# Optimization experiments

Hardware: AMD Instinct MI355X
Metric: run time of the kernel (lower is better)

Reference implementation:

```python
import jax, jax.numpy as jnp
import numpy as np

D = 1024
B = 16384

def setup_inputs() -> dict:
    key = jax.random.key(0)
    ks = jax.random.split(key, 8)
    s = 1.0 / np.sqrt(D)  # torch Linear default init scale (uniform), use scaled normal
    return {
        "f1": jax.random.normal(ks[0], (B, D), jnp.float32),
        "f2": jax.random.normal(ks[1], (B, D), jnp.float32),
        "Wq": jax.random.normal(ks[2], (D, D), jnp.float32) * s,
        "bq": jax.random.normal(ks[3], (D,), jnp.float32) * s,
        "Wk": jax.random.normal(ks[4], (D, D), jnp.float32) * s,
        "bk": jax.random.normal(ks[5], (D,), jnp.float32) * s,
        "Wv": jax.random.normal(ks[6], (D, D), jnp.float32) * s,
        "bv": jax.random.normal(ks[7], (D,), jnp.float32) * s,
    }

def reference(f1, f2, Wq, bq, Wk, bk, Wv, bv):
    d = f1.shape[-1]
    feats = jnp.stack([f1, f2], axis=1)          # [B, 2, D]
    # nn.Linear: y = x @ W.T + b
    Q = jnp.einsum("bsd,ed->bse", feats, Wq) + bq  # [B, 2, D]
    K = jnp.einsum("bsd,ed->bse", feats, Wk) + bk
    V = jnp.einsum("bsd,ed->bse", feats, Wv) + bv
    scores = jnp.einsum("bse,bte->bst", Q, K) / jnp.sqrt(jnp.asarray(d, feats.dtype))  # [B, 2, 2]
    attn = jax.nn.softmax(scores, axis=-1)
    attended = jnp.einsum("bst,btd->bsd", attn, V)  # [B, 2, D]
    return attended.sum(axis=1)                     # [B, D]
```

## Files before the change

kernel.cpp:

```cpp
#include <hip/hip_runtime.h>
#include <hip/hip_bf16.h>
#include <stdint.h>

typedef unsigned short u16;
typedef __bf16 bf16x8 __attribute__((ext_vector_type(8)));
typedef float f32x4 __attribute__((ext_vector_type(4)));

#define D_DIM 1024
#define B_ROWS 16384
#define M_ROWS 32768
#define BM 128
#define BN 128
#define BK 64

__device__ __forceinline__ u16 f2bs(float f) {
    union { float f; unsigned u; } v; v.f = f;
    unsigned r = v.u + 0x7FFFu + ((v.u >> 16) & 1u);
    return (u16)(r >> 16);
}
__device__ __forceinline__ float bs2f(unsigned bits16) {
    union { unsigned u; float f; } v; v.u = bits16 << 16;
    return v.f;
}
__device__ __forceinline__ float b8x(uint4 q, int e) {
    unsigned w[4] = {q.x, q.y, q.z, q.w};
    return bs2f((w[e >> 1] >> ((unsigned)(e & 1) * 16u)) & 0xFFFFu);
}
__device__ __forceinline__ uint2 pack4(float4 f) {
    uint2 r;
    r.x = (unsigned)f2bs(f.x) | ((unsigned)f2bs(f.y) << 16);
    r.y = (unsigned)f2bs(f.z) | ((unsigned)f2bs(f.w) << 16);
    return r;
}

#define GLD16(gsrc, ldst)                                                      \
    __builtin_amdgcn_global_load_lds(                                          \
        (const __attribute__((address_space(1))) void*)(gsrc),                 \
        (__attribute__((address_space(3))) void*)(ldst), 16, 0, 0)

#define MFMA16(a, b, c) __builtin_amdgcn_mfma_f32_16x16x32_bf16((a), (b), (c), 0, 0, 0)

__global__ __launch_bounds__(256) void prep_all(const float* __restrict__ f1,
                                                const float* __restrict__ f2,
                                                const float* __restrict__ Wq,
                                                const float* __restrict__ Wk,
                                                const float* __restrict__ Wv,
                                                const float* __restrict__ bq,
                                                const float* __restrict__ bk,
                                                u16* __restrict__ X,
                                                u16* __restrict__ WqT,
                                                u16* __restrict__ WkT,
                                                u16* __restrict__ Wvb,
                                                float* __restrict__ u,
                                                float* __restrict__ v,
                                                float* __restrict__ cbuf) {
    const int bid = blockIdx.x;
    if (bid < 2048) {
        const float* in = (bid < 1024) ? Wq : Wk;
        u16* out = (bid < 1024) ? WqT : WkT;
        const int b = bid & 1023;
        __shared__ float lds[32][33];
        const int tx = threadIdx.x & 31;
        const int ty = threadIdx.x >> 5;
        const int r0 = (b >> 5) * 32;
        const int c0 = (b & 31) * 32;
#pragma unroll
        for (int i = 0; i < 4; ++i) {
            int r = ty + i * 8;
            lds[r][tx] = in[(size_t)(r0 + r) * D_DIM + c0 + tx];
        }
        __syncthreads();
#pragma unroll
        for (int i = 0; i < 4; ++i) {
            int r = ty + i * 8;
            out[(size_t)(c0 + r) * D_DIM + r0 + tx] = f2bs(lds[tx][r]);
        }
    } else if (bid < 3072) {
        size_t base = ((size_t)(bid - 2048) * 256 + threadIdx.x) * 4;
        *(uint2*)(Wvb + base) = pack4(*(const float4*)(Wv + base));
    } else if (bid < 3104) {
        const int b = bid - 3072;
        const int dl = threadIdx.x & 31;
        const int fg = threadIdx.x >> 5;
        const int d  = b * 32 + dl;
        float au = 0.f, av = 0.f;
        const int f0 = fg * 128;
        for (int f = f0; f < f0 + 128; ++f) {
            au = fmaf(Wq[(size_t)f * D_DIM + d], bk[f], au);
            av = fmaf(Wk[(size_t)f * D_DIM + d], bq[f], av);
        }
        __shared__ float su[8][32], sv[8][32];
        su[fg][dl] = au; sv[fg][dl] = av;
        __syncthreads();
        if (fg == 0) {
            float a = 0.f, b2 = 0.f;
#pragma unroll
            for (int g = 0; g < 8; ++g) { a += su[g][dl]; b2 += sv[g][dl]; }
            u[d] = a; v[d] = b2;
        }
        if (b == 0) {
            __shared__ float red[256];
            float p = 0.f;
            for (int f = threadIdx.x; f < D_DIM; f += 256) p = fmaf(bq[f], bk[f], p);
            red[threadIdx.x] = p;
            __syncthreads();
            for (int s = 128; s; s >>= 1) {
                if (threadIdx.x < s) red[threadIdx.x] += red[threadIdx.x + s];
                __syncthreads();
            }
            if (threadIdx.x == 0) cbuf[0] = red[0];
        }
    } else {
        size_t i4   = (size_t)(bid - 3104) * 256 + threadIdx.x;
        size_t base = i4 * 4;
        size_t brow = base >> 10;
        size_t col  = base & 1023;
        float4 a = *(const float4*)(f1 + base);
        float4 b = *(const float4*)(f2 + base);
        *(uint2*)(X + (2 * brow) * D_DIM + col)     = pack4(a);
        *(uint2*)(X + (2 * brow + 1) * D_DIM + col) = pack4(b);
    }
}

__global__ __launch_bounds__(256, 3) void gemm_small(const u16* __restrict__ A,
                                                     const u16* __restrict__ W,
                                                     u16* __restrict__ C, int ncols) {
    constexpr int K = D_DIM;
    __shared__ u16 As[BM * BK];
    __shared__ u16 Bs[BN * BK];

    const int cpx  = gridDim.x >> 3;
    const int orig = (blockIdx.x & 7) * cpx + (blockIdx.x >> 3);
    const int nTn = ncols / BN;
    const int m0 = (orig / nTn) * BM, n0 = (orig % nTn) * BN;

    const int tid  = threadIdx.x;
    const int lane = tid & 63;
    const int wave = tid >> 6;
    const int wr = wave >> 1, wc = wave & 1;
    const int lr = lane & 15;
    const int kg = lane >> 4;

    f32x4 acc[4][4] = {};

    const int sr  = tid >> 3;
    const int scs = ((tid & 7) ^ ((tid >> 3) & 7)) * 8;
    const u16* aRow = A + (size_t)(m0 + sr) * K + scs;
    const u16* bRow = W + (size_t)(n0 + sr) * K + scs;
    u16* aDst = As + tid * 8;
    u16* bDst = Bs + tid * 8;

    for (int kt = 0; kt < K; kt += BK) {
#pragma unroll
        for (int i = 0; i < 4; ++i) {
            GLD16(aRow + (size_t)i * 32 * K + kt, aDst + i * 2048);
            GLD16(bRow + (size_t)i * 32 * K + kt, bDst + i * 2048);
        }
        __syncthreads();
#pragma unroll
        for (int kk = 0; kk < 2; ++kk) {
            bf16x8 af[4], bfr[4];
            const int kx = kk * 4 + kg;
#pragma unroll
            for (int mf = 0; mf < 4; ++mf) {
                const int R = wr * 64 + mf * 16 + lr;
                af[mf] = *(const bf16x8*)(As + R * 64 + ((kx ^ (R & 7)) * 8));
            }
#pragma unroll
            for (int nf = 0; nf < 4; ++nf) {
                const int S = wc * 64 + nf * 16 + lr;
                bfr[nf] = *(const bf16x8*)(Bs + S * 64 + ((kx ^ (S & 7)) * 8));
            }
#pragma unroll
            for (int mf = 0; mf < 4; ++mf)
#pragma unroll
                for (int nf = 0; nf < 4; ++nf)
                    acc[mf][nf] = MFMA16(af[mf], bfr[nf], acc[mf][nf]);
        }
        __syncthreads();
    }

    const int cr = (lane >> 4) * 4;
    const int cc = lane & 15;
#pragma unroll
    for (int mf = 0; mf < 4; ++mf)
#pragma unroll
        for (int nf = 0; nf < 4; ++nf) {
            int col = n0 + wc * 64 + nf * 16 + cc;
#pragma unroll
            for (int j = 0; j < 4; ++j) {
                int row = m0 + wr * 64 + mf * 16 + cr + j;
                C[(size_t)row * ncols + col] = f2bs(acc[mf][nf][j]);
            }
        }
}

template<int MODE>
__global__ __launch_bounds__(512, 2) void gemm8p(const u16* __restrict__ A,
                                                 const u16* __restrict__ W,
                                                 const float* __restrict__ bias,
                                                 u16* __restrict__ C,
                                                 float* __restrict__ out,
                                                 int ncols) {
    constexpr int K  = D_DIM;
    constexpr int NT = K / 64;
    __shared__ u16 L[65536];

    const int cpx  = gridDim.x >> 3;
    const int orig = (blockIdx.x & 7) * cpx + (blockIdx.x >> 3);
    const int nTn  = ncols >> 8;
    const int m0 = (orig / nTn) << 8, n0 = (orig % nTn) << 8;

    const int tid  = threadIdx.x;
    const int lane = tid & 63;
    const int wid  = tid >> 6;
    const int wm = wid >> 2, wn = wid & 3;
    const int lr = lane & 15;
    const int kg = lane >> 4;
    const int r7 = lr & 7;
    const int cx0 = ((0 + kg) ^ r7) * 8;
    const int cx1 = ((4 + kg) ^ r7) * 8;
    const int sS  = (wn & 1) * 64;

    const int rb  = tid >> 3;
    const int scs = ((tid & 7) ^ (rb & 7)) * 8;
    const u16* aB = A + (size_t)(m0 + rb) * K + scs;
    const u16* bB = W + (size_t)(n0 + rb) * K + scs;
    u16* aD = L + tid * 8;
    u16* bD = L + 32768 + tid * 8;

#define ST_HALF(tile, h)                                                       \
    {                                                                          \
        const int d_ = (tile) & 1;                                             \
        const size_t ko_ = (size_t)(tile) * 64;                                \
        if ((h) < 2) {                                                         \
            const u16* s_ = aB + (size_t)(h) * 128 * K + ko_;                  \
            u16* t_ = aD + (d_ * 2 + (h)) * 8192;                              \
            GLD16(s_, t_);                                                     \
            GLD16(s_ + (size_t)64 * K, t_ + 4096);                            \
        } else {                                                               \
            const u16* s_ = bB + (size_t)((h) - 2) * 128 * K + ko_;            \
            u16* t_ = bD + (d_ * 2 + ((h) - 2)) * 8192;                        \
            GLD16(s_, t_);                                                     \
            GLD16(s_ + (size_t)64 * K, t_ + 4096);                            \
        }                                                                      \
    }

    f32x4 acc[8][4] = {};
    bf16x8 af[8][2], bf[4][2];

#pragma unroll
    for (int h = 0; h < 4; ++h) ST_HALF(0, h);
#pragma unroll
    for (int h = 0; h < 4; ++h) ST_HALF(1, h);
    asm volatile("s_waitcnt vmcnt(8)" ::: "memory");
    __builtin_amdgcn_s_barrier();

#pragma unroll 2
    for (int t = 0; t < NT; ++t) {
        const int d = t & 1;
        const u16* Ab = L + (d * 2 + wm) * 8192;
        const u16* Bb = L + 32768 + (d * 2 + (wn >> 1)) * 8192;
        const bool more = (t + 2 < NT);

#pragma unroll
        for (int m = 0; m < 4; ++m) {
            const int R = m * 16 + lr;
            af[m][0] = *(const bf16x8*)(Ab + R * 64 + cx0);
            af[m][1] = *(const bf16x8*)(Ab + R * 64 + cx1);
        }
#pragma unroll
        for (int n = 0; n < 2; ++n) {
            const int S = sS + n * 16 + lr;
            bf[n][0] = *(const bf16x8*)(Bb + S * 64 + cx0);
            bf[n][1] = *(const bf16x8*)(Bb + S * 64 + cx1);
        }
        __builtin_amdgcn_s_barrier();
        __builtin_amdgcn_s_setprio(1);
#pragma unroll
        for (int m = 0; m < 4; ++m)
#pragma unroll
            for (int n = 0; n < 2; ++n) {
                acc[m][n] = MFMA16(af[m][0], bf[n][0], acc[m][n]);
                acc[m][n] = MFMA16(af[m][1], bf[n][1], acc[m][n]);
            }
        __builtin_amdgcn_s_setprio(0);
        __builtin_amdgcn_s_barrier();

#pragma unroll
        for (int n = 2; n < 4; ++n) {
            const int S = sS + n * 16 + lr;
            bf[n][0] = *(const bf16x8*)(Bb + S * 64 + cx0);
            bf[n][1] = *(const bf16x8*)(Bb + S * 64 + cx1);
        }
        __builtin_amdgcn_s_barrier();
        __builtin_amdgcn_s_setprio(1);
#pragma unroll
        for (int m = 0; m < 4; ++m)
#pragma unroll
            for (int n = 2; n < 4; ++n) {
                acc[m][n] = MFMA16(af[m][0], bf[n][0], acc[m][n]);
                acc[m][n] = MFMA16(af[m][1], bf[n][1], acc[m][n]);
            }
        __builtin_amdgcn_s_setprio(0);
        __builtin_amdgcn_s_barrier();

#pragma unroll
        for (int m = 4; m < 8; ++m) {
            const int R = m * 16 + lr;
            af[m][0] = *(const bf16x8*)(Ab + R * 64 + cx0);
            af[m][1] = *(const bf16x8*)(Ab + R * 64 + cx1);
        }
        if (more) { ST_HALF(t + 2, 2); ST_HALF(t + 2, 3); }
        __builtin_amdgcn_s_barrier();
        __builtin_amdgcn_s_setprio(1);
#pragma unroll
        for (int m = 4; m < 8; ++m)
#pragma unroll
            for (int n = 0; n < 2; ++n) {
                acc[m][n] = MFMA16(af[m][0], bf[n][0], acc[m][n]);
                acc[m][n] = MFMA16(af[m][1], bf[n][1], acc[m][n]);
            }
        __builtin_amdgcn_s_setprio(0);
        __builtin_amdgcn_s_barrier();

        if (more) { ST_HALF(t + 2, 0); ST_HALF(t + 2, 1); }
        __builtin_amdgcn_s_barrier();
        __builtin_amdgcn_s_setprio(1);
#pragma unroll
        for (int m = 4; m < 8; ++m)
#pragma unroll
            for (int n = 2; n < 4; ++n) {
                acc[m][n] = MFMA16(af[m][0], bf[n][0], acc[m][n]);
                acc[m][n] = MFMA16(af[m][1], bf[n][1], acc[m][n]);
            }
        __builtin_amdgcn_s_setprio(0);
        if (more) asm volatile("s_waitcnt vmcnt(8)" ::: "memory");
        else      asm volatile("s_waitcnt vmcnt(0)" ::: "memory");
        __builtin_amdgcn_s_barrier();
    }
#undef ST_HALF

    const int cr = (lane >> 4) * 4;
    const int cc = lane & 15;
    if constexpr (MODE == 0) {
#pragma unroll
        for (int mf = 0; mf < 8; ++mf)
#pragma unroll
            for (int nf = 0; nf < 4; ++nf) {
                int col = n0 + wn * 64 + nf * 16 + cc;
#pragma unroll
                for (int j = 0; j < 4; ++j) {
                    int row = m0 + wm * 128 + mf * 16 + cr + j;
                    C[(size_t)row * ncols + col] = f2bs(acc[mf][nf][j]);
                }
            }
    } else {
#pragma unroll
        for (int mf = 0; mf < 8; ++mf)
#pragma unroll
            for (int nf = 0; nf < 4; ++nf) {
                int col = n0 + wn * 64 + nf * 16 + cc;
                float bsv = 2.0f * bias[col];
#pragma unroll
                for (int j = 0; j < 4; ++j) {
                    int row = m0 + wm * 128 + mf * 16 + cr + j;
                    out[(size_t)row * ncols + col] = acc[mf][nf][j] + bsv;
                }
            }
    }
}

__global__ __launch_bounds__(256) void scores_z(const u16* __restrict__ X,
                                                const u16* __restrict__ G,
                                                const float* __restrict__ u,
                                                const float* __restrict__ v,
                                                const float* __restrict__ cbuf,
                                                u16* __restrict__ Z) {
    const int wave = threadIdx.x >> 6;
    const int lane = threadIdx.x & 63;
    const size_t b = (size_t)blockIdx.x * 4 + wave;
    const u16* x0p = X + (2 * b) * D_DIM;
    const u16* x1p = x0p + D_DIM;
    const u16* g0p = G + (2 * b) * D_DIM;
    const u16* g1p = g0p + D_DIM;

    float d00 = 0.f, d01 = 0.f, d10 = 0.f, d11 = 0.f;
    float au0 = 0.f, au1 = 0.f, bv0 = 0.f, bv1 = 0.f;
    uint4 x0c[2], x1c[2];
#pragma unroll
    for (int s = 0; s < 2; ++s) {
        const int c = s * 512 + lane * 8;
        x0c[s] = *(const uint4*)(x0p + c);
        x1c[s] = *(const uint4*)(x1p + c);
        uint4 g0 = *(const uint4*)(g0p + c);
        uint4 g1 = *(const uint4*)(g1p + c);
        float4 uuA = *(const float4*)(u + c);
        float4 uuB = *(const float4*)(u + c + 4);
        float4 vvA = *(const float4*)(v + c);
        float4 vvB = *(const float4*)(v + c + 4);
        float uA[8] = {uuA.x, uuA.y, uuA.z, uuA.w, uuB.x, uuB.y, uuB.z, uuB.w};
        float vA[8] = {vvA.x, vvA.y, vvA.z, vvA.w, vvB.x, vvB.y, vvB.z, vvB.w};
#pragma unroll
        for (int e = 0; e < 8; ++e) {
            float a0 = b8x(x0c[s], e), a1 = b8x(x1c[s], e);
            float c0 = b8x(g0, e),     c1 = b8x(g1, e);
            d00 = fmaf(a0, c0, d00); d01 = fmaf(a0, c1, d01);
            d10 = fmaf(a1, c0, d10); d11 = fmaf(a1, c1, d11);
            au0 = fmaf(uA[e], a0, au0); au1 = fmaf(uA[e], a1, au1);
            bv0 = fmaf(vA[e], a0, bv0); bv1 = fmaf(vA[e], a1, bv1);
        }
    }
#pragma unroll
    for (int off = 32; off; off >>= 1) {
        d00 += __shfl_xor(d00, off); d01 += __shfl_xor(d01, off);
        d10 += __shfl_xor(d10, off); d11 += __shfl_xor(d11, off);
        au0 += __shfl_xor(au0, off); au1 += __shfl_xor(au1, off);
        bv0 += __shfl_xor(bv0, off); bv1 += __shfl_xor(bv1, off);
    }
    const float cc0 = cbuf[0];
    const float sc = 1.0f / 32.0f;
    float s00 = (d00 + au0 + bv0 + cc0) * sc;
    float s01 = (d01 + au0 + bv1 + cc0) * sc;
    float s10 = (d10 + au1 + bv0 + cc0) * sc;
    float s11 = (d11 + au1 + bv1 + cc0) * sc;
    float mA = fmaxf(s00, s01);
    float e00 = expf(s00 - mA), e01 = expf(s01 - mA);
    float rA = 1.0f / (e00 + e01);
    float mB = fmaxf(s10, s11);
    float e10 = expf(s10 - mB), e11 = expf(s11 - mB);
    float rB = 1.0f / (e10 + e11);
    const float w0 = e00 * rA + e10 * rB;
    const float w1 = e01 * rA + e11 * rB;

#pragma unroll
    for (int s = 0; s < 2; ++s) {
        const int c = s * 512 + lane * 8;
        float4 lo, hi;
        lo.x = w0 * b8x(x0c[s], 0) + w1 * b8x(x1c[s], 0);
        lo.y = w0 * b8x(x0c[s], 1) + w1 * b8x(x1c[s], 1);
        lo.z = w0 * b8x(x0c[s], 2) + w1 * b8x(x1c[s], 2);
        lo.w = w0 * b8x(x0c[s], 3) + w1 * b8x(x1c[s], 3);
        hi.x = w0 * b8x(x0c[s], 4) + w1 * b8x(x1c[s], 4);
        hi.y = w0 * b8x(x0c[s], 5) + w1 * b8x(x1c[s], 5);
        hi.z = w0 * b8x(x0c[s], 6) + w1 * b8x(x1c[s], 6);
        hi.w = w0 * b8x(x0c[s], 7) + w1 * b8x(x1c[s], 7);
        uint2 pl = pack4(lo), ph = pack4(hi);
        uint4 o; o.x = pl.x; o.y = pl.y; o.z = ph.x; o.w = ph.y;
        *(uint4*)(Z + b * D_DIM + c) = o;
    }
}

extern "C" void kernel_launch(void* const* d_in, const int* in_sizes, int n_in,
                              void* d_out, int out_size, void* d_ws, size_t ws_size,
                              hipStream_t stream) {
    const float* f1 = (const float*)d_in[0];
    const float* f2 = (const float*)d_in[1];
    const float* Wq = (const float*)d_in[2];
    const float* bq = (const float*)d_in[3];
    const float* Wk = (const float*)d_in[4];
    const float* bk = (const float*)d_in[5];
    const float* Wv = (const float*)d_in[6];
    const float* bv = (const float*)d_in[7];
    float* out = (float*)d_out;

    char*   w    = (char*)d_ws;
    u16*    X    = (u16*)w;
    u16*    G    = X + (size_t)M_ROWS * D_DIM;
    u16*    Z    = G + (size_t)M_ROWS * D_DIM;
    u16*    Wvb  = Z + (size_t)B_ROWS * D_DIM;
    u16*    WqT  = Wvb + (size_t)D_DIM * D_DIM;
    u16*    WkT  = WqT + (size_t)D_DIM * D_DIM;
    u16*    Mb   = WkT + (size_t)D_DIM * D_DIM;
    float*  u    = (float*)(Mb + (size_t)D_DIM * D_DIM);
    float*  v    = u + D_DIM;
    float*  cbuf = v + D_DIM;

    prep_all<<<3104 + (B_ROWS * D_DIM / 4) / 256, 256, 0, stream>>>(
        f1, f2, Wq, Wk, Wv, bq, bk, X, WqT, WkT, Wvb, u, v, cbuf);

    gemm_small<<<(D_DIM / BM) * (D_DIM / BN), 256, 0, stream>>>(WqT, WkT, Mb, D_DIM);
    gemm8p<0><<<(M_ROWS / 256) * (D_DIM / 256), 512, 0, stream>>>(
        X, Mb, nullptr, G, nullptr, D_DIM);
    scores_z<<<B_ROWS / 4, 256, 0, stream>>>(X, G, u, v, cbuf, Z);
    gemm8p<1><<<(B_ROWS / 256) * (D_DIM / 256), 512, 0, stream>>>(
        Z, Wvb, bv, nullptr, out, D_DIM);
}
```

Before: 196.8 us.

## Fuse score dot products into GEMM epilogue with atomics, drop G intermediate

The X·M GEMM epilogue now reloads the matching X tile into LDS and reduces per-pair score partials (x·g, u·x, v·x) in registers, accumulating them into a small per-pair buffer via atomics. This removes writing and re-reading the 64 MB bf16 G intermediate. Softmax weights are then computed in a tiny kernel, and Z is formed in a separate elementwise kernel. The cost is extra epilogue work, many atomic adds, a zero-init pass and two extra kernel launches.

Measured after the change: 366.5 us. 1.86x slower.

```diff
diff --git a/kernel.cpp b/kernel.cpp
--- a/kernel.cpp
+++ b/kernel.cpp
@@ -53,7 +53,8 @@
                                                 u16* __restrict__ Wvb,
                                                 float* __restrict__ u,
                                                 float* __restrict__ v,
-                                                float* __restrict__ cbuf) {
+                                                float* __restrict__ cbuf,
+                                                float* __restrict__ sc) {
     const int bid = blockIdx.x;
     if (bid < 2048) {
         const float* in = (bid < 1024) ? Wq : Wk;
@@ -110,8 +111,11 @@
             }
             if (threadIdx.x == 0) cbuf[0] = red[0];
         }
+    } else if (bid < 3232) {
+        size_t idx = (size_t)(bid - 3104) * 256 + threadIdx.x;
+        ((float4*)sc)[idx] = make_float4(0.f, 0.f, 0.f, 0.f);
     } else {
-        size_t i4   = (size_t)(bid - 3104) * 256 + threadIdx.x;
+        size_t i4   = (size_t)(bid - 3232) * 256 + threadIdx.x;
         size_t base = i4 * 4;
         size_t brow = base >> 10;
         size_t col  = base & 1023;
@@ -199,7 +203,9 @@
 __global__ __launch_bounds__(512, 2) void gemm8p(const u16* __restrict__ A,
                                                  const u16* __restrict__ W,
                                                  const float* __restrict__ bias,
-                                                 u16* __restrict__ C,
+                                                 const float* __restrict__ uvec,
+                                                 const float* __restrict__ vvec,
+                                                 float* __restrict__ sc,
                                                  float* __restrict__ out,
                                                  int ncols) {
     constexpr int K  = D_DIM;
@@ -223,9 +229,9 @@
     const int sS  = (wn & 1) * 64;
 
     const int rb  = tid >> 3;
-    const int scs = ((tid & 7) ^ (rb & 7)) * 8;
-    const u16* aB = A + (size_t)(m0 + rb) * K + scs;
-    const u16* bB = W + (size_t)(n0 + rb) * K + scs;
+    const int scsw = ((tid & 7) ^ (rb & 7)) * 8;
+    const u16* aB = A + (size_t)(m0 + rb) * K + scsw;
+    const u16* bB = W + (size_t)(n0 + rb) * K + scsw;
     u16* aD = L + tid * 8;
     u16* bD = L + 32768 + tid * 8;
 
@@ -343,19 +349,8 @@
 
     const int cr = (lane >> 4) * 4;
     const int cc = lane & 15;
-    if constexpr (MODE == 0) {
-#pragma unroll
-        for (int mf = 0; mf < 8; ++mf)
-#pragma unroll
-            for (int nf = 0; nf < 4; ++nf) {
-                int col = n0 + wn * 64 + nf * 16 + cc;
-#pragma unroll
-                for (int j = 0; j < 4; ++j) {
-                    int row = m0 + wm * 128 + mf * 16 + cr + j;
-                    C[(size_t)row * ncols + col] = f2bs(acc[mf][nf][j]);
-                }
-            }
-    } else {
+
+    if constexpr (MODE == 1) {
 #pragma unroll
         for (int mf = 0; mf < 8; ++mf)
 #pragma unroll
@@ -368,87 +363,108 @@
                     out[(size_t)row * ncols + col] = acc[mf][nf][j] + bsv;
                 }
             }
+    } else {
+#pragma unroll
+        for (int i = 0; i < 16; ++i) {
+            const int idx  = i * 512 + tid;
+            const int row  = idx >> 5;
+            const int col8 = (idx & 31) * 8;
+            GLD16(A + (size_t)(m0 + row) * K + n0 + col8, L + row * 256 + col8);
+        }
+        asm volatile("s_waitcnt vmcnt(0)" ::: "memory");
+        __builtin_amdgcn_s_barrier();
+
+        float uu[4], vv[4];
+#pragma unroll
+        for (int nf = 0; nf < 4; ++nf) {
+            const int col = n0 + wn * 64 + nf * 16 + cc;
+            uu[nf] = uvec[col];
+            vv[nf] = vvec[col];
+        }
+
+#pragma unroll
+        for (int mf = 0; mf < 8; ++mf) {
+#pragma unroll
+            for (int jp = 0; jp < 2; ++jp) {
+                const int lrow = wm * 128 + mf * 16 + cr + jp * 2;
+                float d00 = 0.f, d01 = 0.f, d10 = 0.f, d11 = 0.f;
+                float a0 = 0.f, a1 = 0.f, b0 = 0.f, b1 = 0.f;
+#pragma unroll
+                for (int nf = 0; nf < 4; ++nf) {
+                    const int c = wn * 64 + nf * 16 + cc;
+                    float px0 = bs2f(L[lrow * 256 + c]);
+                    float px1 = bs2f(L[(lrow + 1) * 256 + c]);
+                    float g0 = acc[mf][nf][jp * 2 + 0];
+                    float g1 = acc[mf][nf][jp * 2 + 1];
+                    d00 = fmaf(px0, g0, d00); d01 = fmaf(px0, g1, d01);
+                    d10 = fmaf(px1, g0, d10); d11 = fmaf(px1, g1, d11);
+                    a0 = fmaf(uu[nf], px0, a0); a1 = fmaf(uu[nf], px1, a1);
+                    b0 = fmaf(vv[nf], px0, b0); b1 = fmaf(vv[nf], px1, b1);
+                }
+#pragma unroll
+                for (int off = 1; off < 16; off <<= 1) {
+                    d00 += __shfl_xor(d00, off); d01 += __shfl_xor(d01, off);
+                    d10 += __shfl_xor(d10, off); d11 += __shfl_xor(d11, off);
+                    a0  += __shfl_xor(a0,  off); a1  += __shfl_xor(a1,  off);
+                    b0  += __shfl_xor(b0,  off); b1  += __shfl_xor(b1,  off);
+                }
+                if ((lane & 15) == 0) {
+                    const int p = (m0 + lrow) >> 1;
+                    float* s = sc + (size_t)p * 8;
+                    atomicAdd(s + 0, d00); atomicAdd(s + 1, d01);
+                    atomicAdd(s + 2, d10); atomicAdd(s + 3, d11);
+                    atomicAdd(s + 4, a0);  atomicAdd(s + 5, a1);
+                    atomicAdd(s + 6, b0);  atomicAdd(s + 7, b1);
+                }
+            }
+        }
     }
 }
 
-__global__ __launch_bounds__(256) void scores_z(const u16* __restrict__ X,
-                                                const u16* __restrict__ G,
-                                                const float* __restrict__ u,
-                                                const float* __restrict__ v,
-                                                const float* __restrict__ cbuf,
-                                                u16* __restrict__ Z) {
-    const int wave = threadIdx.x >> 6;
-    const int lane = threadIdx.x & 63;
-    const size_t b = (size_t)blockIdx.x * 4 + wave;
-    const u16* x0p = X + (2 * b) * D_DIM;
-    const u16* x1p = x0p + D_DIM;
-    const u16* g0p = G + (2 * b) * D_DIM;
-    const u16* g1p = g0p + D_DIM;
-
-    float d00 = 0.f, d01 = 0.f, d10 = 0.f, d11 = 0.f;
-    float au0 = 0.f, au1 = 0.f, bv0 = 0.f, bv1 = 0.f;
-    uint4 x0c[2], x1c[2];
-#pragma unroll
-    for (int s = 0; s < 2; ++s) {
-        const int c = s * 512 + lane * 8;
-        x0c[s] = *(const uint4*)(x0p + c);
-        x1c[s] = *(const uint4*)(x1p + c);
-        uint4 g0 = *(const uint4*)(g0p + c);
-        uint4 g1 = *(const uint4*)(g1p + c);
-        float4 uuA = *(const float4*)(u + c);
-        float4 uuB = *(const float4*)(u + c + 4);
-        float4 vvA = *(const float4*)(v + c);
-        float4 vvB = *(const float4*)(v + c + 4);
-        float uA[8] = {uuA.x, uuA.y, uuA.z, uuA.w, uuB.x, uuB.y, uuB.z, uuB.w};
-        float vA[8] = {vvA.x, vvA.y, vvA.z, vvA.w, vvB.x, vvB.y, vvB.z, vvB.w};
-#pragma unroll
-        for (int e = 0; e < 8; ++e) {
-            float a0 = b8x(x0c[s], e), a1 = b8x(x1c[s], e);
-            float c0 = b8x(g0, e),     c1 = b8x(g1, e);
-            d00 = fmaf(a0, c0, d00); d01 = fmaf(a0, c1, d01);
-            d10 = fmaf(a1, c0, d10); d11 = fmaf(a1, c1, d11);
-            au0 = fmaf(uA[e], a0, au0); au1 = fmaf(uA[e], a1, au1);
-            bv0 = fmaf(vA[e], a0, bv0); bv1 = fmaf(vA[e], a1, bv1);
-        }
-    }
-#pragma unroll
-    for (int off = 32; off; off >>= 1) {
-        d00 += __shfl_xor(d00, off); d01 += __shfl_xor(d01, off);
-        d10 += __shfl_xor(d10, off); d11 += __shfl_xor(d11, off);
-        au0 += __shfl_xor(au0, off); au1 += __shfl_xor(au1, off);
-        bv0 += __shfl_xor(bv0, off); bv1 += __shfl_xor(bv1, off);
-    }
-    const float cc0 = cbuf[0];
-    const float sc = 1.0f / 32.0f;
-    float s00 = (d00 + au0 + bv0 + cc0) * sc;
-    float s01 = (d01 + au0 + bv1 + cc0) * sc;
-    float s10 = (d10 + au1 + bv0 + cc0) * sc;
-    float s11 = (d11 + au1 + bv1 + cc0) * sc;
+__global__ __launch_bounds__(256) void wts_k(const float* __restrict__ sc,
+                                             const float* __restrict__ cbuf,
+                                             float2* __restrict__ wts) {
+    const int p = blockIdx.x * 256 + threadIdx.x;
+    const float* s = sc + (size_t)p * 8;
+    const float c0 = cbuf[0];
+    const float scl = 1.0f / 32.0f;
+    float s00 = (s[0] + s[4] + s[6] + c0) * scl;
+    float s01 = (s[1] + s[4] + s[7] + c0) * scl;
+    float s10 = (s[2] + s[5] + s[6] + c0) * scl;
+    float s11 = (s[3] + s[5] + s[7] + c0) * scl;
     float mA = fmaxf(s00, s01);
     float e00 = expf(s00 - mA), e01 = expf(s01 - mA);
     float rA = 1.0f / (e00 + e01);
     float mB = fmaxf(s10, s11);
     float e10 = expf(s10 - mB), e11 = expf(s11 - mB);
     float rB = 1.0f / (e10 + e11);
-    const float w0 = e00 * rA + e10 * rB;
-    const float w1 = e01 * rA + e11 * rB;
-
-#pragma unroll
-    for (int s = 0; s < 2; ++s) {
-        const int c = s * 512 + lane * 8;
-        float4 lo, hi;
-        lo.x = w0 * b8x(x0c[s], 0) + w1 * b8x(x1c[s], 0);
-        lo.y = w0 * b8x(x0c[s], 1) + w1 * b8x(x1c[s], 1);
-        lo.z = w0 * b8x(x0c[s], 2) + w1 * b8x(x1c[s], 2);
-        lo.w = w0 * b8x(x0c[s], 3) + w1 * b8x(x1c[s], 3);
-        hi.x = w0 * b8x(x0c[s], 4) + w1 * b8x(x1c[s], 4);
-        hi.y = w0 * b8x(x0c[s], 5) + w1 * b8x(x1c[s], 5);
-        hi.z = w0 * b8x(x0c[s], 6) + w1 * b8x(x1c[s], 6);
-        hi.w = w0 * b8x(x0c[s], 7) + w1 * b8x(x1c[s], 7);
-        uint2 pl = pack4(lo), ph = pack4(hi);
-        uint4 o; o.x = pl.x; o.y = pl.y; o.z = ph.x; o.w = ph.y;
-        *(uint4*)(Z + b * D_DIM + c) = o;
-    }
+    float2 w;
+    w.x = e00 * rA + e10 * rB;
+    w.y = e01 * rA + e11 * rB;
+    wts[p] = w;
+}
+
+__global__ __launch_bounds__(256) void z_k(const u16* __restrict__ X,
+                                           const float2* __restrict__ wts,
+                                           u16* __restrict__ Z) {
+    const size_t idx = (size_t)blockIdx.x * 256 + threadIdx.x;
+    const size_t b   = idx >> 7;
+    const int    c   = (int)(idx & 127) * 8;
+    const float2 w = wts[b];
+    uint4 x0 = *(const uint4*)(X + (2 * b) * D_DIM + c);
+    uint4 x1 = *(const uint4*)(X + (2 * b + 1) * D_DIM + c);
+    float4 lo, hi;
+    lo.x = w.x * b8x(x0, 0) + w.y * b8x(x1, 0);
+    lo.y = w.x * b8x(x0, 1) + w.y * b8x(x1, 1);
+    lo.z = w.x * b8x(x0, 2) + w.y * b8x(x1, 2);
+    lo.w = w.x * b8x(x0, 3) + w.y * b8x(x1, 3);
+    hi.x = w.x * b8x(x0, 4) + w.y * b8x(x1, 4);
+    hi.y = w.x * b8x(x0, 5) + w.y * b8x(x1, 5);
+    hi.z = w.x * b8x(x0, 6) + w.y * b8x(x1, 6);
+    hi.w = w.x * b8x(x0, 7) + w.y * b8x(x1, 7);
+    uint2 pl = pack4(lo), ph = pack4(hi);
+    uint4 o; o.x = pl.x; o.y = pl.y; o.z = ph.x; o.w = ph.y;
+    *(uint4*)(Z + b * D_DIM + c) = o;
 }
 
 extern "C" void kernel_launch(void* const* d_in, const int* in_sizes, int n_in,
@@ -466,8 +482,7 @@
 
     char*   w    = (char*)d_ws;
     u16*    X    = (u16*)w;
-    u16*    G    = X + (size_t)M_ROWS * D_DIM;
-    u16*    Z    = G + (size_t)M_ROWS * D_DIM;
+    u16*    Z    = X + (size_t)M_ROWS * D_DIM;
     u16*    Wvb  = Z + (size_t)B_ROWS * D_DIM;
     u16*    WqT  = Wvb + (size_t)D_DIM * D_DIM;
     u16*    WkT  = WqT + (size_t)D_DIM * D_DIM;
@@ -475,14 +490,17 @@
     float*  u    = (float*)(Mb + (size_t)D_DIM * D_DIM);
     float*  v    = u + D_DIM;
     float*  cbuf = v + D_DIM;
-
-    prep_all<<<3104 + (B_ROWS * D_DIM / 4) / 256, 256, 0, stream>>>(
-        f1, f2, Wq, Wk, Wv, bq, bk, X, WqT, WkT, Wvb, u, v, cbuf);
+    float*  sc   = cbuf + 64;
+    float2* wts  = (float2*)(sc + (size_t)B_ROWS * 8);
+
+    prep_all<<<3232 + (B_ROWS * D_DIM / 4) / 256, 256, 0, stream>>>(
+        f1, f2, Wq, Wk, Wv, bq, bk, X, WqT, WkT, Wvb, u, v, cbuf, sc);
 
     gemm_small<<<(D_DIM / BM) * (D_DIM / BN), 256, 0, stream>>>(WqT, WkT, Mb, D_DIM);
-    gemm8p<0><<<(M_ROWS / 256) * (D_DIM / 256), 512, 0, stream>>>(
-        X, Mb, nullptr, G, nullptr, D_DIM);
-    scores_z<<<B_ROWS / 4, 256, 0, stream>>>(X, G, u, v, cbuf, Z);
+    gemm8p<2><<<(M_ROWS / 256) * (D_DIM / 256), 512, 0, stream>>>(
+        X, Mb, nullptr, u, v, sc, nullptr, D_DIM);
+    wts_k<<<B_ROWS / 256, 256, 0, stream>>>(sc, cbuf, wts);
+    z_k<<<(B_ROWS * D_DIM / 8) / 256, 256, 0, stream>>>(X, wts, Z);
     gemm8p<1><<<(B_ROWS / 256) * (D_DIM / 256), 512, 0, stream>>>(
-        Z, Wvb, bv, nullptr, out, D_DIM);
-}
+        Z, Wvb, bv, nullptr, nullptr, nullptr, out, D_DIM);
+}
```
